# Kernel optimization log

Hardware: AMD Instinct MI355X
Metric: run time of the kernel (lower is better)

Reference implementation:

```python
import jax, jax.numpy as jnp
import numpy as np

VOCAB, EMBED, HIDDEN, NUM_OUT = 50000, 256, 64, 16
BATCH, T = 64, 2048
BN_EPS = 1e-5


def setup_inputs() -> dict:
    key = jax.random.key(0)
    ks = jax.random.split(key, 12)
    x = jax.random.randint(ks[0], (BATCH, T), 0, VOCAB, dtype=jnp.int64)
    seq_lengths = jax.random.randint(ks[1], (BATCH,), 1, T, dtype=jnp.int64)
    emb = jax.random.normal(ks[2], (VOCAB, EMBED), dtype=jnp.float32) * 0.1
    emb = emb.at[0].set(0.0)  # padding_idx=0
    s_ih = 1.0 / np.sqrt(HIDDEN)
    W_ih = jax.random.uniform(ks[3], (4 * HIDDEN, EMBED), jnp.float32, -s_ih, s_ih)
    W_hh = jax.random.uniform(ks[4], (4 * HIDDEN, HIDDEN), jnp.float32, -s_ih, s_ih)
    b_ih = jax.random.uniform(ks[5], (4 * HIDDEN,), jnp.float32, -s_ih, s_ih)
    b_hh = jax.random.uniform(ks[6], (4 * HIDDEN,), jnp.float32, -s_ih, s_ih)
    bn_gamma = jnp.ones((HIDDEN,), jnp.float32)
    bn_beta = jnp.zeros((HIDDEN,), jnp.float32)
    bn_mean = jnp.zeros((HIDDEN,), jnp.float32)
    bn_var = jnp.ones((HIDDEN,), jnp.float32)
    s_fc = 1.0 / np.sqrt(HIDDEN)
    fc_w = jax.random.uniform(ks[7], (NUM_OUT, HIDDEN), jnp.float32, -s_fc, s_fc)
    fc_b = jax.random.uniform(ks[8], (NUM_OUT,), jnp.float32, -s_fc, s_fc)
    return {"x": x, "seq_lengths": seq_lengths, "emb": emb, "W_ih": W_ih,
            "W_hh": W_hh, "b_ih": b_ih, "b_hh": b_hh, "bn_gamma": bn_gamma,
            "bn_beta": bn_beta, "bn_mean": bn_mean, "bn_var": bn_var,
            "fc_w": fc_w, "fc_b": fc_b}


def reference(x, seq_lengths, emb, W_ih, W_hh, b_ih, b_hh,
              bn_gamma, bn_beta, bn_mean, bn_var, fc_w, fc_b):
    B, Tn = x.shape
    H = W_hh.shape[1]
    x_embed = emb[x]                       # [B, T, E] (dropout is identity in eval)
    xe_t = jnp.transpose(x_embed, (1, 0, 2))  # [T, B, E] time-major for scan
    # precompute input projections for all timesteps in one big GEMM
    gx = jnp.einsum('tbe,ge->tbg', xe_t, W_ih) + b_ih + b_hh  # [T, B, 4H]

    def step(carry, gxt):
        h, c = carry
        gates = gxt + h @ W_hh.T           # [B, 4H]
        i, f, g, o = jnp.split(gates, 4, axis=-1)  # torch LSTMCell gate order
        i = jax.nn.sigmoid(i)
        f = jax.nn.sigmoid(f)
        g = jnp.tanh(g)
        o = jax.nn.sigmoid(o)
        c = f * c + i * g
        h = o * jnp.tanh(c)
        return (h, c), None

    h0 = jnp.zeros((B, H), x_embed.dtype)
    c0 = jnp.zeros((B, H), x_embed.dtype)
    (h_last, _), _ = jax.lax.scan(step, (h0, c0), gx)
    # BatchNorm1d (eval mode: running stats)
    h_bn = (h_last - bn_mean) * jax.lax.rsqrt(bn_var + BN_EPS) * bn_gamma + bn_beta
    return h_bn @ fc_w.T + fc_b            # [B, num_output]
```

## Files before the change

kernel.cpp:

```cpp
#include <hip/hip_runtime.h>
#include <math.h>

#define VOCAB   50000
#define EMBED   256
#define HIDDEN  64
#define G4      256
#define BATCH   64
#define TSEQ    2048
#define NUM_OUT 16

typedef _Float16 h2 __attribute__((ext_vector_type(2)));

__device__ __forceinline__ float fexp2f(float x) { return __builtin_amdgcn_exp2f(x); }
__device__ __forceinline__ float frcpf(float x)  { return __builtin_amdgcn_rcpf(x); }

__device__ __forceinline__ float dot2(h2 a, h2 b, float c) {
#if __has_builtin(__builtin_amdgcn_fdot2)
    return __builtin_amdgcn_fdot2(a, b, c, false);
#else
    float r;
    asm("v_dot2_f32_f16 %0, %1, %2, %3"
        : "=v"(r)
        : "v"(__builtin_bit_cast(int, a)), "v"(__builtin_bit_cast(int, b)), "v"(c));
    return r;
#endif
}

template <int CTRL>
__device__ __forceinline__ float dppf(float v) {
    return __int_as_float(__builtin_amdgcn_update_dpp(
        0, __float_as_int(v), CTRL, 0xF, 0xF, true));
}

#define REP32(M) M(0) M(1) M(2) M(3) M(4) M(5) M(6) M(7) \
                 M(8) M(9) M(10) M(11) M(12) M(13) M(14) M(15) \
                 M(16) M(17) M(18) M(19) M(20) M(21) M(22) M(23) \
                 M(24) M(25) M(26) M(27) M(28) M(29) M(30) M(31)

__global__ __launch_bounds__(256) void proj_kernel(
    const float* __restrict__ emb, const float* __restrict__ W_ih,
    const float* __restrict__ b_ih, const float* __restrict__ b_hh,
    float* __restrict__ proj)
{
    __shared__ __align__(16) float As[64][68];
    __shared__ __align__(16) float Bs[64][68];

    const int tid = threadIdx.x;
    const int R0 = blockIdx.x * 64;
    const int G0 = blockIdx.y * 64;

    const int rr = (tid & 15) * 4;
    const int gg = (tid >> 4) * 4;

    float acc[4][4] = {};

    for (int kc = 0; kc < 4; ++kc) {
        #pragma unroll
        for (int it = 0; it < 4; ++it) {
            int flat = (it * 256 + tid) * 4;
            int r = flat >> 6;
            int k = flat & 63;
            int row = R0 + r;
            float4 v = make_float4(0.f, 0.f, 0.f, 0.f);
            if (row < VOCAB)
                v = *(const float4*)&emb[(size_t)row * EMBED + kc * 64 + k];
            As[k + 0][r] = v.x; As[k + 1][r] = v.y;
            As[k + 2][r] = v.z; As[k + 3][r] = v.w;
            float4 wv = *(const float4*)&W_ih[(size_t)(G0 + r) * EMBED + kc * 64 + k];
            Bs[k + 0][r] = wv.x; Bs[k + 1][r] = wv.y;
            Bs[k + 2][r] = wv.z; Bs[k + 3][r] = wv.w;
        }
        __syncthreads();

        #pragma unroll 8
        for (int k = 0; k < 64; ++k) {
            float4 a = *(const float4*)&As[k][rr];
            float4 b = *(const float4*)&Bs[k][gg];
            acc[0][0] = fmaf(a.x, b.x, acc[0][0]);
            acc[0][1] = fmaf(a.x, b.y, acc[0][1]);
            acc[0][2] = fmaf(a.x, b.z, acc[0][2]);
            acc[0][3] = fmaf(a.x, b.w, acc[0][3]);
            acc[1][0] = fmaf(a.y, b.x, acc[1][0]);
            acc[1][1] = fmaf(a.y, b.y, acc[1][1]);
            acc[1][2] = fmaf(a.y, b.z, acc[1][2]);
            acc[1][3] = fmaf(a.y, b.w, acc[1][3]);
            acc[2][0] = fmaf(a.z, b.x, acc[2][0]);
            acc[2][1] = fmaf(a.z, b.y, acc[2][1]);
            acc[2][2] = fmaf(a.z, b.z, acc[2][2]);
            acc[2][3] = fmaf(a.z, b.w, acc[2][3]);
            acc[3][0] = fmaf(a.w, b.x, acc[3][0]);
            acc[3][1] = fmaf(a.w, b.y, acc[3][1]);
            acc[3][2] = fmaf(a.w, b.z, acc[3][2]);
            acc[3][3] = fmaf(a.w, b.w, acc[3][3]);
        }
        __syncthreads();
    }

    float bias[4];
    #pragma unroll
    for (int v = 0; v < 4; ++v)
        bias[v] = b_ih[G0 + gg + v] + b_hh[G0 + gg + v];

    #pragma unroll
    for (int u = 0; u < 4; ++u) {
        int row = R0 + rr + u;
        if (row < VOCAB) {
            float4 o;
            o.x = acc[u][0] + bias[0];
            o.y = acc[u][1] + bias[1];
            o.z = acc[u][2] + bias[2];
            o.w = acc[u][3] + bias[3];
            *(float4*)&proj[(size_t)row * G4 + G0 + gg] = o;
        }
    }
}

__global__ __launch_bounds__(256) void lstm_scan(
    const int* __restrict__ x, const float* __restrict__ proj,
    const float* __restrict__ W_hh,
    const float* __restrict__ bn_gamma, const float* __restrict__ bn_beta,
    const float* __restrict__ bn_mean, const float* __restrict__ bn_var,
    const float* __restrict__ fc_w, const float* __restrict__ fc_b,
    float* __restrict__ out)
{
    const int b   = blockIdx.x;
    const int tid = threadIdx.x;
    const int w   = tid >> 6;
    const int l   = tid & 63;
    const int q   = l & 3;
    const int unit = w * 16 + (l >> 2);

    __shared__ int   toks[TSEQ];
    __shared__ __align__(16) short hbuf[2][HIDDEN];
    __shared__ float hfin[HIDDEN];
    __shared__ float hb_s[HIDDEN];

    for (int i = tid; i < TSEQ; i += 256) toks[i] = x[b * TSEQ + i];
    if (tid < 2 * HIDDEN) ((short*)hbuf)[tid] = 0;

    const float* Wr = &W_hh[(size_t)(q * HIDDEN + unit) * HIDDEN];
#define WR_DECL(n) h2 wr##n;
    REP32(WR_DECL)
#undef WR_DECL
#define WR_LOAD(n) { float2 v = *(const float2*)&Wr[2 * (n)]; \
                     wr##n = h2{(_Float16)v.x, (_Float16)v.y}; }
    REP32(WR_LOAD)
#undef WR_LOAD

    const float s_k = (q == 2) ? 2.8853900817779268f : 1.4426950408889634f;
    const float s_m = (q == 2) ? 2.0f : 1.0f;
    const bool qodd = (q & 1) != 0;
    const bool qhi  = (q & 2) != 0;

    float c = 0.0f, hmy = 0.0f;
    const float* projw = proj + q * HIDDEN + unit;

    __syncthreads();

    float gx0 = projw[(size_t)toks[0] * G4];
    float gx1 = projw[(size_t)toks[1] * G4];
    float gx2 = projw[(size_t)toks[2] * G4];
    float gx3 = projw[(size_t)toks[3] * G4];
    int tk0 = toks[4], tk1 = toks[5], tk2 = toks[6], tk3 = toks[7];

#define DOTG(R, W0, W1, W2, W3) \
    a0 = dot2(W0, __builtin_bit_cast(h2, R.x), a0); \
    a1 = dot2(W1, __builtin_bit_cast(h2, R.y), a1); \
    a2 = dot2(W2, __builtin_bit_cast(h2, R.z), a2); \
    a3 = dot2(W3, __builtin_bit_cast(h2, R.w), a3);

#define STEP(RP, WP, GX, TK, TTOK) { \
     \
    const int4* hp = (const int4*)hbuf[RP]; \
    int4 r0 = hp[0], r1 = hp[1], r2 = hp[2], r3 = hp[3]; \
    int4 r4 = hp[4], r5 = hp[5], r6 = hp[6], r7 = hp[7]; \
     \
    int tnew = toks[(TTOK) + 8 < TSEQ ? (TTOK) + 8 : TSEQ - 1]; \
    float gnew = projw[(size_t)(TK) * G4]; \
    float a0 = 0.f, a1 = 0.f, a2 = 0.f, a3 = 0.f; \
    DOTG(r0, wr0,  wr1,  wr2,  wr3)  DOTG(r1, wr4,  wr5,  wr6,  wr7) \
    DOTG(r2, wr8,  wr9,  wr10, wr11) DOTG(r3, wr12, wr13, wr14, wr15) \
    DOTG(r4, wr16, wr17, wr18, wr19) DOTG(r5, wr20, wr21, wr22, wr23) \
    DOTG(r6, wr24, wr25, wr26, wr27) DOTG(r7, wr28, wr29, wr30, wr31) \
    float gv = ((a0 + a1) + (a2 + a3)) + GX;    \
    GX = gnew; TK = tnew; \
    float tt = fexp2f(s_k * gv); \
    float rr = 1.0f - s_m * frcpf(tt + 1.0f);             \
    float b1 = dppf<0xB1>(rr);                            \
    float b2 = dppf<0x4E>(rr);                            \
    float b3 = dppf<0x1B>(rr);                            \
    float A  = qodd ? b1 : rr,  B  = qodd ? b3 : b2; \
    float A2 = qodd ? rr : b1,  B2 = qodd ? b2 : b3; \
    float i_ = qhi ? B  : A,    g_ = qhi ? A  : B; \
    float f_ = qhi ? B2 : A2,   o_ = qhi ? A2 : B2; \
    c = fmaf(f_, c, i_ * g_); \
    float e2 = fexp2f(2.8853900817779268f * c); \
    float th = 1.0f - 2.0f * frcpf(e2 + 1.0f);            \
    hmy = o_ * th; \
    if (q == 0) hbuf[WP][unit] = __builtin_bit_cast(short, (_Float16)hmy); \
    asm volatile("s_waitcnt lgkmcnt(0)" ::: "memory"); \
    __builtin_amdgcn_s_barrier(); \
}

    for (int t = 0; t < TSEQ; t += 4) {
        STEP(0, 1, gx0, tk0, t)
        STEP(1, 0, gx1, tk1, t + 1)
        STEP(0, 1, gx2, tk2, t + 2)
        STEP(1, 0, gx3, tk3, t + 3)
    }
#undef STEP
#undef DOTG

    if (q == 0) hfin[unit] = hmy;
    __syncthreads();
    if (tid < HIDDEN) {
        float hb = (hfin[tid] - bn_mean[tid]) * rsqrtf(bn_var[tid] + 1e-5f)
                   * bn_gamma[tid] + bn_beta[tid];
        hb_s[tid] = hb;
    }
    __syncthreads();
    if (tid < NUM_OUT) {
        float s0 = fc_b[tid], s1 = 0.f, s2 = 0.f, s3 = 0.f;
        #pragma unroll
        for (int k = 0; k < HIDDEN; k += 4) {
            s0 = fmaf(hb_s[k + 0], fc_w[tid * HIDDEN + k + 0], s0);
            s1 = fmaf(hb_s[k + 1], fc_w[tid * HIDDEN + k + 1], s1);
            s2 = fmaf(hb_s[k + 2], fc_w[tid * HIDDEN + k + 2], s2);
            s3 = fmaf(hb_s[k + 3], fc_w[tid * HIDDEN + k + 3], s3);
        }
        out[b * NUM_OUT + tid] = (s0 + s1) + (s2 + s3);
    }
}

extern "C" void kernel_launch(void* const* d_in, const int* in_sizes, int n_in,
                              void* d_out, int out_size, void* d_ws, size_t ws_size,
                              hipStream_t stream) {
    const int*   x        = (const int*)d_in[0];
    const float* emb      = (const float*)d_in[2];
    const float* W_ih     = (const float*)d_in[3];
    const float* W_hh     = (const float*)d_in[4];
    const float* b_ih     = (const float*)d_in[5];
    const float* b_hh     = (const float*)d_in[6];
    const float* bn_gamma = (const float*)d_in[7];
    const float* bn_beta  = (const float*)d_in[8];
    const float* bn_mean  = (const float*)d_in[9];
    const float* bn_var   = (const float*)d_in[10];
    const float* fc_w     = (const float*)d_in[11];
    const float* fc_b     = (const float*)d_in[12];

    float* proj = (float*)d_ws;

    dim3 pgrid((VOCAB + 63) / 64, G4 / 64);
    proj_kernel<<<pgrid, 256, 0, stream>>>(emb, W_ih, b_ih, b_hh, proj);

    lstm_scan<<<BATCH, 256, 0, stream>>>(x, proj, W_hh,
                                         bn_gamma, bn_beta, bn_mean, bn_var,
                                         fc_w, fc_b, (float*)d_out);
}
```

Baseline: 652.3 us.

## Use MFMA fp16 for vocab projection and fold exp2 scaling into weights

Replaces the FP32 LDS-tiled vocab projection GEMM with an MFMA 16x16x32 fp16 kernel that reads embedding and W_ih rows straight from global memory, converts them to fp16, and writes the projected table pre-scaled by log2e factors. The recurrent weights are pre-scaled the same way, so each scan step skips the per-gate multiply before exp2. The precomputed gate input seeds the dot accumulator, and the tanh/sigmoid tails are rewritten as fmas. Token padding removes the index clamp. This trades fp16 rounding of the embedding projection for fewer instructions on the serial critical path and a cheaper projection pass.

```diff
diff --git a/kernel.cpp b/kernel.cpp
--- a/kernel.cpp
+++ b/kernel.cpp
@@ -9,7 +9,12 @@
 #define TSEQ    2048
 #define NUM_OUT 16
 
-typedef _Float16 h2 __attribute__((ext_vector_type(2)));
+typedef _Float16 h2   __attribute__((ext_vector_type(2)));
+typedef _Float16 f16x8 __attribute__((ext_vector_type(8)));
+typedef float    f32x4 __attribute__((ext_vector_type(4)));
+
+#define LOG2E  1.4426950408889634f
+#define LOG2E2 2.8853900817779268f
 
 __device__ __forceinline__ float fexp2f(float x) { return __builtin_amdgcn_exp2f(x); }
 __device__ __forceinline__ float frcpf(float x)  { return __builtin_amdgcn_rcpf(x); }
@@ -37,80 +42,61 @@
                  M(16) M(17) M(18) M(19) M(20) M(21) M(22) M(23) \
                  M(24) M(25) M(26) M(27) M(28) M(29) M(30) M(31)
 
-__global__ __launch_bounds__(256) void proj_kernel(
+__global__ __launch_bounds__(256) void proj_mfma(
     const float* __restrict__ emb, const float* __restrict__ W_ih,
     const float* __restrict__ b_ih, const float* __restrict__ b_hh,
     float* __restrict__ proj)
 {
-    __shared__ __align__(16) float As[64][68];
-    __shared__ __align__(16) float Bs[64][68];
-
-    const int tid = threadIdx.x;
-    const int R0 = blockIdx.x * 64;
-    const int G0 = blockIdx.y * 64;
-
-    const int rr = (tid & 15) * 4;
-    const int gg = (tid >> 4) * 4;
-
-    float acc[4][4] = {};
-
-    for (int kc = 0; kc < 4; ++kc) {
+    const int tid  = threadIdx.x;
+    const int w    = tid >> 6;
+    const int lane = tid & 63;
+    const int R0   = blockIdx.x * 64;
+
+    const int rowA  = R0 + w * 16 + (lane & 15);
+    const int rowAc = rowA < VOCAB ? rowA : VOCAB - 1;
+    const int kb    = (lane >> 4) * 8;
+    const float* arow = emb + (size_t)rowAc * EMBED + kb;
+
+    f32x4 acc[16];
+    #pragma unroll
+    for (int t = 0; t < 16; ++t) acc[t] = f32x4{0.f, 0.f, 0.f, 0.f};
+
+    #pragma unroll
+    for (int kc = 0; kc < 8; ++kc) {
+        float4 alo = *(const float4*)(arow + kc * 32);
+        float4 ahi = *(const float4*)(arow + kc * 32 + 4);
+        f16x8 af;
+        af[0] = (_Float16)alo.x; af[1] = (_Float16)alo.y;
+        af[2] = (_Float16)alo.z; af[3] = (_Float16)alo.w;
+        af[4] = (_Float16)ahi.x; af[5] = (_Float16)ahi.y;
+        af[6] = (_Float16)ahi.z; af[7] = (_Float16)ahi.w;
         #pragma unroll
-        for (int it = 0; it < 4; ++it) {
-            int flat = (it * 256 + tid) * 4;
-            int r = flat >> 6;
-            int k = flat & 63;
-            int row = R0 + r;
-            float4 v = make_float4(0.f, 0.f, 0.f, 0.f);
+        for (int t = 0; t < 16; ++t) {
+            const float* brow = W_ih + (size_t)(t * 16 + (lane & 15)) * EMBED
+                                + kc * 32 + kb;
+            float4 blo = *(const float4*)brow;
+            float4 bhi = *(const float4*)(brow + 4);
+            f16x8 bf;
+            bf[0] = (_Float16)blo.x; bf[1] = (_Float16)blo.y;
+            bf[2] = (_Float16)blo.z; bf[3] = (_Float16)blo.w;
+            bf[4] = (_Float16)bhi.x; bf[5] = (_Float16)bhi.y;
+            bf[6] = (_Float16)bhi.z; bf[7] = (_Float16)bhi.w;
+            acc[t] = __builtin_amdgcn_mfma_f32_16x16x32_f16(af, bf, acc[t], 0, 0, 0);
+        }
+    }
+
+    const int crow0 = R0 + w * 16 + (lane >> 4) * 4;
+    const int colin = lane & 15;
+    #pragma unroll
+    for (int t = 0; t < 16; ++t) {
+        int g = t * 16 + colin;
+        float bias = b_ih[g] + b_hh[g];
+        float sc = ((g >> 6) == 2) ? LOG2E2 : LOG2E;
+        #pragma unroll
+        for (int j = 0; j < 4; ++j) {
+            int row = crow0 + j;
             if (row < VOCAB)
-                v = *(const float4*)&emb[(size_t)row * EMBED + kc * 64 + k];
-            As[k + 0][r] = v.x; As[k + 1][r] = v.y;
-            As[k + 2][r] = v.z; As[k + 3][r] = v.w;
-            float4 wv = *(const float4*)&W_ih[(size_t)(G0 + r) * EMBED + kc * 64 + k];
-            Bs[k + 0][r] = wv.x; Bs[k + 1][r] = wv.y;
-            Bs[k + 2][r] = wv.z; Bs[k + 3][r] = wv.w;
-        }
-        __syncthreads();
-
-        #pragma unroll 8
-        for (int k = 0; k < 64; ++k) {
-            float4 a = *(const float4*)&As[k][rr];
-            float4 b = *(const float4*)&Bs[k][gg];
-            acc[0][0] = fmaf(a.x, b.x, acc[0][0]);
-            acc[0][1] = fmaf(a.x, b.y, acc[0][1]);
-            acc[0][2] = fmaf(a.x, b.z, acc[0][2]);
-            acc[0][3] = fmaf(a.x, b.w, acc[0][3]);
-            acc[1][0] = fmaf(a.y, b.x, acc[1][0]);
-            acc[1][1] = fmaf(a.y, b.y, acc[1][1]);
-            acc[1][2] = fmaf(a.y, b.z, acc[1][2]);
-            acc[1][3] = fmaf(a.y, b.w, acc[1][3]);
-            acc[2][0] = fmaf(a.z, b.x, acc[2][0]);
-            acc[2][1] = fmaf(a.z, b.y, acc[2][1]);
-            acc[2][2] = fmaf(a.z, b.z, acc[2][2]);
-            acc[2][3] = fmaf(a.z, b.w, acc[2][3]);
-            acc[3][0] = fmaf(a.w, b.x, acc[3][0]);
-            acc[3][1] = fmaf(a.w, b.y, acc[3][1]);
-            acc[3][2] = fmaf(a.w, b.z, acc[3][2]);
-            acc[3][3] = fmaf(a.w, b.w, acc[3][3]);
-        }
-        __syncthreads();
-    }
-
-    float bias[4];
-    #pragma unroll
-    for (int v = 0; v < 4; ++v)
-        bias[v] = b_ih[G0 + gg + v] + b_hh[G0 + gg + v];
-
-    #pragma unroll
-    for (int u = 0; u < 4; ++u) {
-        int row = R0 + rr + u;
-        if (row < VOCAB) {
-            float4 o;
-            o.x = acc[u][0] + bias[0];
-            o.y = acc[u][1] + bias[1];
-            o.z = acc[u][2] + bias[2];
-            o.w = acc[u][3] + bias[3];
-            *(float4*)&proj[(size_t)row * G4 + G0 + gg] = o;
+                proj[(size_t)row * G4 + g] = (acc[t][j] + bias) * sc;
         }
     }
 }
@@ -130,25 +116,27 @@
     const int q   = l & 3;
     const int unit = w * 16 + (l >> 2);
 
-    __shared__ int   toks[TSEQ];
+    __shared__ int   toks[TSEQ + 8];
     __shared__ __align__(16) short hbuf[2][HIDDEN];
     __shared__ float hfin[HIDDEN];
     __shared__ float hb_s[HIDDEN];
 
-    for (int i = tid; i < TSEQ; i += 256) toks[i] = x[b * TSEQ + i];
+    for (int i = tid; i < TSEQ + 8; i += 256)
+        toks[i] = x[b * TSEQ + (i < TSEQ ? i : TSEQ - 1)];
     if (tid < 2 * HIDDEN) ((short*)hbuf)[tid] = 0;
 
+    const float s_k = (q == 2) ? LOG2E2 : LOG2E;
     const float* Wr = &W_hh[(size_t)(q * HIDDEN + unit) * HIDDEN];
 #define WR_DECL(n) h2 wr##n;
     REP32(WR_DECL)
 #undef WR_DECL
 #define WR_LOAD(n) { float2 v = *(const float2*)&Wr[2 * (n)]; \
-                     wr##n = h2{(_Float16)v.x, (_Float16)v.y}; }
+                     wr##n = h2{(_Float16)(v.x * s_k), (_Float16)(v.y * s_k)}; }
     REP32(WR_LOAD)
 #undef WR_LOAD
 
-    const float s_k = (q == 2) ? 2.8853900817779268f : 1.4426950408889634f;
-    const float s_m = (q == 2) ? 2.0f : 1.0f;
+    const float s_c = (q == 2) ? LOG2E2 : 1.0f;
+    const float s_m = (q == 2) ? 2.0f * LOG2E2 : 1.0f;
     const bool qodd = (q & 1) != 0;
     const bool qhi  = (q & 2) != 0;
 
@@ -163,29 +151,29 @@
     float gx3 = projw[(size_t)toks[3] * G4];
     int tk0 = toks[4], tk1 = toks[5], tk2 = toks[6], tk3 = toks[7];
 
+    const int4* hp0 = (const int4*)hbuf[0];
+    const int4* hp1 = (const int4*)hbuf[1];
+
 #define DOTG(R, W0, W1, W2, W3) \
     a0 = dot2(W0, __builtin_bit_cast(h2, R.x), a0); \
     a1 = dot2(W1, __builtin_bit_cast(h2, R.y), a1); \
     a2 = dot2(W2, __builtin_bit_cast(h2, R.z), a2); \
     a3 = dot2(W3, __builtin_bit_cast(h2, R.w), a3);
 
-#define STEP(RP, WP, GX, TK, TTOK) { \
-     \
-    const int4* hp = (const int4*)hbuf[RP]; \
-    int4 r0 = hp[0], r1 = hp[1], r2 = hp[2], r3 = hp[3]; \
-    int4 r4 = hp[4], r5 = hp[5], r6 = hp[6], r7 = hp[7]; \
-     \
-    int tnew = toks[(TTOK) + 8 < TSEQ ? (TTOK) + 8 : TSEQ - 1]; \
+#define STEP(HP, WB, GX, TK, TT) { \
+    int4 r0 = (HP)[0], r1 = (HP)[1], r2 = (HP)[2], r3 = (HP)[3]; \
+    int4 r4 = (HP)[4], r5 = (HP)[5], r6 = (HP)[6], r7 = (HP)[7]; \
+    int tnew = toks[(TT) + 8]; \
     float gnew = projw[(size_t)(TK) * G4]; \
-    float a0 = 0.f, a1 = 0.f, a2 = 0.f, a3 = 0.f; \
+    float a0 = GX, a1 = 0.f, a2 = 0.f, a3 = 0.f; \
     DOTG(r0, wr0,  wr1,  wr2,  wr3)  DOTG(r1, wr4,  wr5,  wr6,  wr7) \
     DOTG(r2, wr8,  wr9,  wr10, wr11) DOTG(r3, wr12, wr13, wr14, wr15) \
     DOTG(r4, wr16, wr17, wr18, wr19) DOTG(r5, wr20, wr21, wr22, wr23) \
     DOTG(r6, wr24, wr25, wr26, wr27) DOTG(r7, wr28, wr29, wr30, wr31) \
-    float gv = ((a0 + a1) + (a2 + a3)) + GX;    \
+    float gv = (a0 + a1) + (a2 + a3); \
     GX = gnew; TK = tnew; \
-    float tt = fexp2f(s_k * gv); \
-    float rr = 1.0f - s_m * frcpf(tt + 1.0f);             \
+    float tt2 = fexp2f(gv); \
+    float rr = fmaf(-s_m, frcpf(tt2 + 1.0f), s_c);        \
     float b1 = dppf<0xB1>(rr);                            \
     float b2 = dppf<0x4E>(rr);                            \
     float b3 = dppf<0x1B>(rr);                            \
@@ -193,20 +181,22 @@
     float A2 = qodd ? rr : b1,  B2 = qodd ? b2 : b3; \
     float i_ = qhi ? B  : A,    g_ = qhi ? A  : B; \
     float f_ = qhi ? B2 : A2,   o_ = qhi ? A2 : B2; \
-    c = fmaf(f_, c, i_ * g_); \
-    float e2 = fexp2f(2.8853900817779268f * c); \
-    float th = 1.0f - 2.0f * frcpf(e2 + 1.0f);            \
-    hmy = o_ * th; \
-    if (q == 0) hbuf[WP][unit] = __builtin_bit_cast(short, (_Float16)hmy); \
+    float o2 = o_ + o_; \
+    c = fmaf(f_, c, i_ * g_);                             \
+    float e2 = fexp2f(c); \
+    float rv = frcpf(e2 + 1.0f); \
+    hmy = fmaf(-o2, rv, o_);                              \
+    if (q == 0) hbuf[WB][unit] = __builtin_bit_cast(short, (_Float16)hmy); \
     asm volatile("s_waitcnt lgkmcnt(0)" ::: "memory"); \
     __builtin_amdgcn_s_barrier(); \
+    asm volatile("" ::: "memory"); \
 }
 
     for (int t = 0; t < TSEQ; t += 4) {
-        STEP(0, 1, gx0, tk0, t)
-        STEP(1, 0, gx1, tk1, t + 1)
-        STEP(0, 1, gx2, tk2, t + 2)
-        STEP(1, 0, gx3, tk3, t + 3)
+        STEP(hp0, 1, gx0, tk0, t)
+        STEP(hp1, 0, gx1, tk1, t + 1)
+        STEP(hp0, 1, gx2, tk2, t + 2)
+        STEP(hp1, 0, gx3, tk3, t + 3)
     }
 #undef STEP
 #undef DOTG
@@ -250,8 +240,7 @@
 
     float* proj = (float*)d_ws;
 
-    dim3 pgrid((VOCAB + 63) / 64, G4 / 64);
-    proj_kernel<<<pgrid, 256, 0, stream>>>(emb, W_ih, b_ih, b_hh, proj);
+    proj_mfma<<<(VOCAB + 63) / 64, 256, 0, stream>>>(emb, W_ih, b_ih, b_hh, proj);
 
     lstm_scan<<<BATCH, 256, 0, stream>>>(x, proj, W_hh,
                                          bn_gamma, bn_beta, bn_mean, bn_var,
```

Measured after the change: 715.4 us. 1.1x slower.
